# Kernel tuning notes

Hardware: AMD Instinct MI355X
Metric: run time of the kernel (lower is better)

Reference implementation:

```python
import jax, jax.numpy as jnp
import numpy as np

B, L, D = 4, 2048, 512
DK = D // 2
DH = 256.0  # scaling denominator


def _skew(QE):
    # QE: [B, L, M] with M == L (relative position logits via skewing trick)
    b, l, m = QE.shape
    pad = jnp.zeros((b, l, 1), QE.dtype)
    cat = jnp.concatenate([pad, QE], axis=2)      # [B, L, M+1]
    reshaped = cat.reshape(b, m + 1, l)           # [B, M+1, L]
    return reshaped[:, 1:, :]                     # [B, M, L]


def setup_inputs() -> dict:
    key = jax.random.key(0)
    ks = jax.random.split(key, 7)
    return {
        "inputQ": jax.random.normal(ks[0], (B, L, D), jnp.float32),
        "inputK": jax.random.normal(ks[1], (B, L, D), jnp.float32),
        "inputV": jax.random.normal(ks[2], (B, L, D), jnp.float32),
        "Wq": jax.random.normal(ks[3], (D, DK), jnp.float32) * 0.02,
        "Wk": jax.random.normal(ks[4], (D, DK), jnp.float32) * 0.02,
        "Wv": jax.random.normal(ks[5], (D, D), jnp.float32) * 0.02,
        "E": jax.random.normal(ks[6], (L, DK), jnp.float32) * 0.02,
    }


def reference(inputQ, inputK, inputV, Wq, Wk, Wv, E):
    Q = jnp.einsum('bld,dk->blk', inputQ, Wq)   # [B, L, DK]
    K = jnp.einsum('bld,dk->blk', inputK, Wk)   # [B, L, DK]
    V = jnp.einsum('bld,de->ble', inputV, Wv)   # [B, L, D]
    QE = jnp.einsum('blk,mk->blm', Q, E)        # [B, L, max_seq]
    Srel = _skew(QE)                             # [B, L, L]
    QKt = jnp.einsum('blk,bmk->blm', Q, K)      # [B, L, L]
    attn = jax.nn.softmax((QKt + Srel) / jnp.sqrt(jnp.float32(DH)), axis=-1)
    return jnp.einsum('blm,bme->ble', attn, V)  # [B, L, D]
```

## Files before the change

### kernel.cpp

```cpp
#include <hip/hip_runtime.h>
#include <hip/hip_bf16.h>

#define BB 4
#define LL 2048
#define DD 512
#define DKK 256

typedef __bf16 bf16;
typedef __bf16 bf16x4 __attribute__((ext_vector_type(4)));
typedef __bf16 bf16x8 __attribute__((ext_vector_type(8)));
typedef float f32x4 __attribute__((ext_vector_type(4)));

__device__ __forceinline__ void async_ld16(const bf16* g, bf16* l) {
    __builtin_amdgcn_global_load_lds(
        (const __attribute__((address_space(1))) void*)g,
        (__attribute__((address_space(3))) void*)l, 16, 0, 0);
}

__global__ void conv3_f32_bf16(const float* __restrict__ a, const float* __restrict__ bq,
                               const float* __restrict__ c,
                               bf16* __restrict__ oa, bf16* __restrict__ ob,
                               bf16* __restrict__ oc, int n4) {
    const float* in = (blockIdx.y == 0) ? a : (blockIdx.y == 1) ? bq : c;
    bf16* out = (blockIdx.y == 0) ? oa : (blockIdx.y == 1) ? ob : oc;
    int i = blockIdx.x * 256 + threadIdx.x;
    if (i < n4) {
        f32x4 v = *(const f32x4*)(in + (size_t)i * 4);
        bf16x4 o;
        #pragma unroll
        for (int j = 0; j < 4; ++j) o[j] = (bf16)v[j];
        *(bf16x4*)(out + (size_t)i * 4) = o;
    }
}

__global__ void prep_misc(const float* __restrict__ E, const float* __restrict__ Wq,
                          const float* __restrict__ Wk, const float* __restrict__ Wv,
                          bf16* __restrict__ Eb, bf16* __restrict__ WqT,
                          bf16* __restrict__ WkT, bf16* __restrict__ WvT) {
    int y = blockIdx.y;
    int idx = blockIdx.x * 256 + threadIdx.x;
    if (y == 0) {
        if (idx < (LL * DKK) / 4) {
            f32x4 v = *(const f32x4*)(E + (size_t)idx * 4);
            bf16x4 o;
            #pragma unroll
            for (int j = 0; j < 4; ++j) o[j] = (bf16)v[j];
            *(bf16x4*)(Eb + (size_t)idx * 4) = o;
        }
    } else if (y == 1) {
        if (idx < DD * DKK) { int r = idx / DKK, c = idx % DKK; WqT[(size_t)c * DD + r] = (bf16)Wq[idx]; }
    } else if (y == 2) {
        if (idx < DD * DKK) { int r = idx / DKK, c = idx % DKK; WkT[(size_t)c * DD + r] = (bf16)Wk[idx]; }
    } else {
        if (idx < DD * DD)  { int r = idx / DD,  c = idx % DD;  WvT[(size_t)c * DD + r] = (bf16)Wv[idx]; }
    }
}

__launch_bounds__(256, 2)
__global__ void gemm_qkv(const bf16* __restrict__ Xq, const bf16* __restrict__ WqT,
                         bf16* __restrict__ Qw,
                         const bf16* __restrict__ Xk, const bf16* __restrict__ WkT,
                         bf16* __restrict__ Kw,
                         const bf16* __restrict__ Xv, const bf16* __restrict__ WvT,
                         bf16* __restrict__ Vt)
{
    __shared__ bf16 Als[2][128 * 32];
    __shared__ bf16 Bls[2][128 * 32];
    __shared__ bf16 tbuf[64 * 136];

    int tid  = threadIdx.x;
    int lane = tid & 63;
    int wid  = tid >> 6;
    int l15  = lane & 15;
    int quad = lane >> 4;

    int bid  = blockIdx.x;
    int mode = (bid < 128) ? 0 : (bid < 256) ? 1 : 2;
    int idx  = bid - ((mode == 0) ? 0 : (mode == 1) ? 128 : 256);
    int nb   = (mode == 2) ? 4 : 2;
    int gx = idx % nb;
    int gy = idx / nb;
    int N  = (mode == 2) ? DD : DKK;
    const bf16* A  = (mode == 0) ? Xq  : (mode == 1) ? Xk  : Xv;
    const bf16* Bw = (mode == 0) ? WqT : (mode == 1) ? WkT : WvT;
    const int K = DD;

    const bf16* Ab = A + (size_t)gy * 128 * K;
    const bf16* Bb = Bw + (size_t)gx * 128 * K;

    int rl = lane >> 2;
    int sl = lane & 3;
    int half = wid & 1;
    const bf16* gsrc = (wid < 2) ? Ab : Bb;
    bf16* ldst0 = (wid < 2) ? Als[0] : Bls[0];
    bf16* ldst1 = (wid < 2) ? Als[1] : Bls[1];

    const bf16* gptr[4];
    #pragma unroll
    for (int u = 0; u < 4; ++u) {
        int inst = half * 4 + u;
        int row  = inst * 16 + rl;
        int c    = (sl - (row >> 1)) & 3;
        gptr[u] = gsrc + (size_t)row * K + c * 8;
    }

    f32x4 acc[4][4];
    #pragma unroll
    for (int i = 0; i < 4; ++i)
        #pragma unroll
        for (int j = 0; j < 4; ++j) acc[i][j] = 0;

    for (int k0 = 0; k0 < K; k0 += 64) {
        #pragma unroll
        for (int u = 0; u < 4; ++u) {
            async_ld16(gptr[u],      ldst0 + (half * 4 + u) * 512);
            async_ld16(gptr[u] + 32, ldst1 + (half * 4 + u) * 512);
            gptr[u] += 64;
        }
        __syncthreads();
        #pragma unroll
        for (int h2 = 0; h2 < 2; ++h2) {
            bf16x8 fA[4], fB[4];
            #pragma unroll
            for (int rt = 0; rt < 4; ++rt) {
                int row = (wid & 1) * 64 + rt * 16 + l15;
                int s   = (quad + (row >> 1)) & 3;
                fA[rt] = *(const bf16x8*)&Als[h2][row * 32 + s * 8];
            }
            #pragma unroll
            for (int ct = 0; ct < 4; ++ct) {
                int col = (wid >> 1) * 64 + ct * 16 + l15;
                int s   = (quad + (col >> 1)) & 3;
                fB[ct] = *(const bf16x8*)&Bls[h2][col * 32 + s * 8];
            }
            #pragma unroll
            for (int rt = 0; rt < 4; ++rt)
                #pragma unroll
                for (int ct = 0; ct < 4; ++ct)
                    acc[rt][ct] = __builtin_amdgcn_mfma_f32_16x16x32_bf16(
                                      fA[rt], fB[ct], acc[rt][ct], 0, 0, 0);
        }
        __syncthreads();
    }

    if (mode == 2) {
        #pragma unroll
        for (int p = 0; p < 2; ++p) {
            if ((wid >> 1) == p) {
                #pragma unroll
                for (int rt = 0; rt < 4; ++rt)
                    #pragma unroll
                    for (int ct = 0; ct < 4; ++ct)
                        #pragma unroll
                        for (int r = 0; r < 4; ++r)
                            tbuf[(ct * 16 + l15) * 136
                                 + (wid & 1) * 64 + rt * 16 + quad * 4 + r]
                                = (bf16)acc[rt][ct][r];
            }
            __syncthreads();
            int row = tid >> 2, c0 = (tid & 3) * 32;
            bf16* dst = Vt + (size_t)(gx * 128 + p * 64 + row) * (BB * LL)
                           + (size_t)gy * 128 + c0;
            #pragma unroll
            for (int q = 0; q < 4; ++q)
                *(bf16x8*)(dst + q * 8) = *(const bf16x8*)&tbuf[row * 136 + c0 + q * 8];
            __syncthreads();
        }
    } else {
        bf16* Cb = (mode == 0) ? Qw : Kw;
        int m0 = gy * 128 + (wid & 1) * 64;
        int n0 = gx * 128 + (wid >> 1) * 64;
        #pragma unroll
        for (int rt = 0; rt < 4; ++rt)
            #pragma unroll
            for (int ct = 0; ct < 4; ++ct)
                #pragma unroll
                for (int r = 0; r < 4; ++r) {
                    int m = m0 + rt * 16 + quad * 4 + r;
                    int n = n0 + ct * 16 + l15;
                    Cb[(size_t)m * N + n] = (bf16)acc[rt][ct][r];
                }
    }
}

__launch_bounds__(256, 2)
__global__ void gemm_srel(const bf16* __restrict__ A, const bf16* __restrict__ B,
                          bf16* __restrict__ C, long aStride, long cStride)
{
    __shared__ bf16 Als[2][128 * 32];
    __shared__ bf16 Bls[2][128 * 32];

    int tid  = threadIdx.x;
    int lane = tid & 63;
    int wid  = tid >> 6;
    int l15  = lane & 15;
    int quad = lane >> 4;
    const int N = LL, K = DKK;
    int nb = N >> 7;
    int gx = blockIdx.x % nb;
    int gy = blockIdx.x / nb;

    const bf16* Ab = A + (size_t)blockIdx.y * aStride + (size_t)gy * 128 * K;
    const bf16* Bb = B + (size_t)gx * 128 * K;

    int rl = lane >> 2;
    int sl = lane & 3;
    int half = wid & 1;
    const bf16* gsrc = (wid < 2) ? Ab : Bb;
    bf16* ldst0 = (wid < 2) ? Als[0] : Bls[0];
    bf16* ldst1 = (wid < 2) ? Als[1] : Bls[1];

    const bf16* gptr[4];
    #pragma unroll
    for (int u = 0; u < 4; ++u) {
        int inst = half * 4 + u;
        int row  = inst * 16 + rl;
        int c    = (sl - (row >> 1)) & 3;
        gptr[u] = gsrc + (size_t)row * K + c * 8;
    }

    f32x4 acc[4][4];
    #pragma unroll
    for (int i = 0; i < 4; ++i)
        #pragma unroll
        for (int j = 0; j < 4; ++j) acc[i][j] = 0;

    for (int k0 = 0; k0 < K; k0 += 64) {
        #pragma unroll
        for (int u = 0; u < 4; ++u) {
            async_ld16(gptr[u],      ldst0 + (half * 4 + u) * 512);
            async_ld16(gptr[u] + 32, ldst1 + (half * 4 + u) * 512);
            gptr[u] += 64;
        }
        __syncthreads();
        #pragma unroll
        for (int h2 = 0; h2 < 2; ++h2) {
            bf16x8 fA[4], fB[4];
            #pragma unroll
            for (int rt = 0; rt < 4; ++rt) {
                int row = (wid & 1) * 64 + rt * 16 + l15;
                int s   = (quad + (row >> 1)) & 3;
                fA[rt] = *(const bf16x8*)&Als[h2][row * 32 + s * 8];
            }
            #pragma unroll
            for (int ct = 0; ct < 4; ++ct) {
                int col = (wid >> 1) * 64 + ct * 16 + l15;
                int s   = (quad + (col >> 1)) & 3;
                fB[ct] = *(const bf16x8*)&Bls[h2][col * 32 + s * 8];
            }
            #pragma unroll
            for (int rt = 0; rt < 4; ++rt)
                #pragma unroll
                for (int ct = 0; ct < 4; ++ct)
                    acc[rt][ct] = __builtin_amdgcn_mfma_f32_16x16x32_bf16(
                                      fA[rt], fB[ct], acc[rt][ct], 0, 0, 0);
        }
        __syncthreads();
    }

    bf16* Cb = C + (size_t)blockIdx.y * cStride;
    int m0 = gy * 128 + (wid & 1) * 64;
    int n0 = gx * 128 + (wid >> 1) * 64;
    #pragma unroll
    for (int rt = 0; rt < 4; ++rt)
        #pragma unroll
        for (int ct = 0; ct < 4; ++ct)
            #pragma unroll
            for (int r = 0; r < 4; ++r) {
                int row = m0 + rt * 16 + quad * 4 + r;
                int c   = n0 + ct * 16 + l15;
                bool lower = (c >= LL - 1 - row);
                int dr = lower ? row : row - 1;
                int dc = lower ? c - (LL - 1 - row) : c + row + 1;
                if (lower || row >= 1)
                    Cb[(size_t)dr * LL + dc] = (bf16)acc[rt][ct][r];
            }
}

__launch_bounds__(256, 2)
__global__ void attn_kernel(const bf16* __restrict__ Qw, const bf16* __restrict__ Kw,
                            const bf16* __restrict__ Vt, const bf16* __restrict__ Srel,
                            float* __restrict__ out)
{
    __shared__ bf16  Klds[64 * 256];
    __shared__ bf16  Vlds[256 * 64];
    __shared__ float Ss[32][68];
    __shared__ bf16  Ps[32][72];
    __shared__ float mSt[32], lSt[32], aSt[32];

    int tid  = threadIdx.x;
    int lane = tid & 63;
    int wid  = tid >> 6;
    int l15  = lane & 15;
    int quad = lane >> 4;

    int xcd = blockIdx.x & 7;
    int b   = xcd >> 1;
    int dh  = xcd & 1;
    int i0  = (blockIdx.x >> 3) * 32;

    const bf16* Qb = Qw + (size_t)b * LL * DKK;
    const bf16* Kb = Kw + (size_t)b * LL * DKK;
    const bf16* Sb = Srel + (size_t)b * LL * LL;
    const bf16* Vb = Vt + (size_t)(dh * 256) * (BB * LL) + (size_t)b * LL;

    const bf16* kptr[8];
    const bf16* vptr[8];
    #pragma unroll
    for (int u = 0; u < 8; ++u) {
        int inst = wid * 8 + u;
        int j_ = inst * 2 + (lane >> 5);
        int ck = ((lane & 31) - j_) & 31;
        kptr[u] = Kb + (size_t)j_ * DKK + ck * 8;
        int d_ = inst * 8 + (lane >> 3);
        int cv = ((lane & 7) - d_) & 7;
        vptr[u] = Vb + (size_t)d_ * (BB * LL) + cv * 8;
    }

    bf16x8 Qreg[2][8];
    #pragma unroll
    for (int rt = 0; rt < 2; ++rt)
        #pragma unroll
        for (int ks = 0; ks < 8; ++ks)
            Qreg[rt][ks] = *(const bf16x8*)(Qb + (size_t)(i0 + rt * 16 + l15) * DKK
                                            + ks * 32 + quad * 8);

    if (tid < 32) { mSt[tid] = -1e30f; lSt[tid] = 0.f; }

    f32x4 accO[2][4];
    #pragma unroll
    for (int rt = 0; rt < 2; ++rt)
        #pragma unroll
        for (int nt = 0; nt < 4; ++nt) accO[rt][nt] = 0;

    asm volatile("s_waitcnt vmcnt(0)" ::: "memory");

    #pragma unroll
    for (int u = 0; u < 8; ++u) {
        async_ld16(kptr[u], Klds + (wid * 8 + u) * 512);
        kptr[u] += 64 * DKK;
    }
    __builtin_amdgcn_sched_barrier(0);
    int srow = i0 + (tid >> 3), ssg = tid & 7;
    bf16x8 srelCur = *(const bf16x8*)(Sb + (size_t)srow * LL + ssg * 8);
    const bf16* sPtr = Sb + (size_t)srow * LL + ssg * 8 + 64;
    __builtin_amdgcn_sched_barrier(0);
    #pragma unroll
    for (int u = 0; u < 8; ++u) {
        async_ld16(vptr[u], Vlds + (wid * 8 + u) * 512);
        vptr[u] += 64;
    }

    int jrow = wid * 16 + l15;

    for (int j0 = 0; j0 < LL; j0 += 64) {
        bool notlast = (j0 + 64 < LL);

        asm volatile("s_waitcnt vmcnt(9)" ::: "memory");
        bf16x8 kf[8];
        #pragma unroll
        for (int ks = 0; ks < 8; ++ks) {
            int cp = (ks * 4 + quad + jrow) & 31;
            kf[ks] = *(const bf16x8*)&Klds[jrow * 256 + cp * 8];
        }
        asm volatile("s_waitcnt lgkmcnt(0)" ::: "memory");
        __builtin_amdgcn_sched_barrier(0);
        if (notlast) {
            #pragma unroll
            for (int u = 0; u < 8; ++u) {
                async_ld16(kptr[u], Klds + (wid * 8 + u) * 512);
                kptr[u] += 64 * DKK;
            }
        }
        __builtin_amdgcn_sched_barrier(0);
        bf16x8 srelNext;
        if (notlast) {
            srelNext = *(const bf16x8*)sPtr;
            sPtr += 64;
        }
        __builtin_amdgcn_sched_barrier(0);
        f32x4 s0 = 0, s1 = 0;
        __builtin_amdgcn_s_setprio(1);
        #pragma unroll
        for (int ks = 0; ks < 8; ++ks) {
            s0 = __builtin_amdgcn_mfma_f32_16x16x32_bf16(Qreg[0][ks], kf[ks], s0, 0, 0, 0);
            s1 = __builtin_amdgcn_mfma_f32_16x16x32_bf16(Qreg[1][ks], kf[ks], s1, 0, 0, 0);
        }
        __builtin_amdgcn_s_setprio(0);
        #pragma unroll
        for (int r = 0; r < 4; ++r) {
            Ss[quad * 4 + r][wid * 16 + l15]      = s0[r];
            Ss[16 + quad * 4 + r][wid * 16 + l15] = s1[r];
        }
        asm volatile("s_waitcnt lgkmcnt(0)\ns_barrier" ::: "memory");

        {
            int r = tid >> 3, sg = tid & 7;
            int i = i0 + r;
            float v[8];
            #pragma unroll
            for (int c = 0; c < 8; ++c) {
                float sr = (j0 + sg * 8 + c == i + 1) ? 0.f : (float)srelCur[c];
                v[c] = (Ss[r][sg * 8 + c] + sr) * 0.0625f;
            }
            float tmax = v[0];
            #pragma unroll
            for (int c = 1; c < 8; ++c) tmax = fmaxf(tmax, v[c]);
            tmax = fmaxf(tmax, __shfl_xor(tmax, 1));
            tmax = fmaxf(tmax, __shfl_xor(tmax, 2));
            tmax = fmaxf(tmax, __shfl_xor(tmax, 4));
            float mOld = mSt[r], lOld = lSt[r];
            float mNew = fmaxf(mOld, tmax);
            float alpha = __expf(mOld - mNew);
            float ps = 0.f;
            bf16x8 pv;
            #pragma unroll
            for (int c = 0; c < 8; ++c) {
                float p = __expf(v[c] - mNew);
                ps += p;
                pv[c] = (bf16)p;
            }
            ps += __shfl_xor(ps, 1);
            ps += __shfl_xor(ps, 2);
            ps += __shfl_xor(ps, 4);
            *(bf16x8*)&Ps[r][sg * 8] = pv;
            if (sg == 0) { mSt[r] = mNew; lSt[r] = alpha * lOld + ps; aSt[r] = alpha; }
        }
        srelCur = srelNext;
        asm volatile("s_waitcnt lgkmcnt(0)\ns_barrier" ::: "memory");

        if (notlast) asm volatile("s_waitcnt vmcnt(9)" ::: "memory");
        else         asm volatile("s_waitcnt vmcnt(0)" ::: "memory");
        bf16x8 aF[2][2];
        #pragma unroll
        for (int rt = 0; rt < 2; ++rt)
            #pragma unroll
            for (int kk = 0; kk < 2; ++kk)
                aF[rt][kk] = *(const bf16x8*)&Ps[rt * 16 + l15][kk * 32 + quad * 8];
        float ar[2][4];
        #pragma unroll
        for (int rt = 0; rt < 2; ++rt)
            #pragma unroll
            for (int r = 0; r < 4; ++r) ar[rt][r] = aSt[rt * 16 + quad * 4 + r];
        bf16x8 vf[4][2];
        #pragma unroll
        for (int nt = 0; nt < 4; ++nt) {
            int dd = wid * 64 + nt * 16 + l15;
            int c0 = (quad + dd) & 7;
            int c1 = (4 + quad + dd) & 7;
            vf[nt][0] = *(const bf16x8*)&Vlds[dd * 64 + c0 * 8];
            vf[nt][1] = *(const bf16x8*)&Vlds[dd * 64 + c1 * 8];
        }
        asm volatile("s_waitcnt lgkmcnt(0)" ::: "memory");
        __builtin_amdgcn_sched_barrier(0);
        if (notlast) {
            #pragma unroll
            for (int u = 0; u < 8; ++u) {
                async_ld16(vptr[u], Vlds + (wid * 8 + u) * 512);
                vptr[u] += 64;
            }
        }
        __builtin_amdgcn_sched_barrier(0);
        __builtin_amdgcn_s_setprio(1);
        #pragma unroll
        for (int nt = 0; nt < 4; ++nt) {
            #pragma unroll
            for (int rt = 0; rt < 2; ++rt) {
                f32x4 o = accO[rt][nt];
                o[0] *= ar[rt][0]; o[1] *= ar[rt][1];
                o[2] *= ar[rt][2]; o[3] *= ar[rt][3];
                o = __builtin_amdgcn_mfma_f32_16x16x32_bf16(aF[rt][0], vf[nt][0], o, 0, 0, 0);
                o = __builtin_amdgcn_mfma_f32_16x16x32_bf16(aF[rt][1], vf[nt][1], o, 0, 0, 0);
                accO[rt][nt] = o;
            }
        }
        __builtin_amdgcn_s_setprio(0);
    }
    float lr[2][4];
    #pragma unroll
    for (int rt = 0; rt < 2; ++rt)
        #pragma unroll
        for (int r = 0; r < 4; ++r) lr[rt][r] = 1.f / lSt[rt * 16 + quad * 4 + r];
    #pragma unroll
    for (int rt = 0; rt < 2; ++rt)
        #pragma unroll
        for (int nt = 0; nt < 4; ++nt)
            #pragma unroll
            for (int r = 0; r < 4; ++r) {
                int i = i0 + rt * 16 + quad * 4 + r;
                int d = dh * 256 + wid * 64 + nt * 16 + l15;
                out[((size_t)b * LL + i) * DD + d] = accO[rt][nt][r] * lr[rt][r];
            }
}

extern "C" void kernel_launch(void* const* d_in, const int* in_sizes, int n_in,
                              void* d_out, int out_size, void* d_ws, size_t ws_size,
                              hipStream_t stream) {
    const float* inQ = (const float*)d_in[0];
    const float* inK = (const float*)d_in[1];
    const float* inV = (const float*)d_in[2];
    const float* Wq  = (const float*)d_in[3];
    const float* Wk  = (const float*)d_in[4];
    const float* Wv  = (const float*)d_in[5];
    const float* E   = (const float*)d_in[6];
    float* out = (float*)d_out;

    char* ws = (char*)d_ws;
    bf16* Qw   = (bf16*)(ws);
    bf16* Kw   = (bf16*)(ws + ((size_t)4  << 20));
    bf16* Vt   = (bf16*)(ws + ((size_t)8  << 20));
    bf16* SrelW= (bf16*)(ws + ((size_t)16 << 20));
    bf16* Xq   = (bf16*)(ws + ((size_t)16 << 20));
    bf16* Xk   = (bf16*)(ws + ((size_t)24 << 20));
    bf16* Xv   = (bf16*)(ws + ((size_t)32 << 20));
    bf16* WqT  = (bf16*)(ws + ((size_t)48 << 20));
    bf16* WkT  = (bf16*)(ws + ((size_t)48 << 20) + 262144);
    bf16* WvT  = (bf16*)(ws + ((size_t)48 << 20) + 524288);
    bf16* Eb   = (bf16*)(ws + ((size_t)49 << 20));

    conv3_f32_bf16<<<dim3(4096, 3), 256, 0, stream>>>(inQ, inK, inV, Xq, Xk, Xv,
                                                      (BB * LL * DD) / 4);
    prep_misc<<<dim3(1024, 4), 256, 0, stream>>>(E, Wq, Wk, Wv, Eb, WqT, WkT, WvT);

    gemm_qkv<<<512, 256, 0, stream>>>(Xq, WqT, Qw, Xk, WkT, Kw, Xv, WvT, Vt);
    gemm_srel<<<dim3(16 * 16, BB), 256, 0, stream>>>(Qw, Eb, SrelW,
                                                     (long)LL * DKK, (long)LL * LL);
    attn_kernel<<<dim3(BB * 64 * 2), 256, 0, stream>>>(Qw, Kw, Vt, SrelW, out);
}
```

Before: 221.7 us.

## Double-buffer LDS in projection and Srel GEMMs; merge prep kernels into one launch

The QKV and Srel GEMMs now use two LDS stages, so the async global-to-LDS load for the next K-slice is issued before the MFMA work on the current slice, and one barrier per step is removed. The two conversion/transpose prep kernels are combined into a single launch that dispatches on block index. This roughly doubles LDS use per block (the V transpose buffer now aliases the A stage buffer), which may lower occupancy. Correctness depends on the async LDS loads having landed by the next barrier.

Result: faster. 211.6 us (-4.5%).

```diff
diff --git a/kernel.cpp b/kernel.cpp
--- a/kernel.cpp
+++ b/kernel.cpp
@@ -17,42 +17,46 @@
         (__attribute__((address_space(3))) void*)l, 16, 0, 0);
 }
 
-__global__ void conv3_f32_bf16(const float* __restrict__ a, const float* __restrict__ bq,
-                               const float* __restrict__ c,
-                               bf16* __restrict__ oa, bf16* __restrict__ ob,
-                               bf16* __restrict__ oc, int n4) {
-    const float* in = (blockIdx.y == 0) ? a : (blockIdx.y == 1) ? bq : c;
-    bf16* out = (blockIdx.y == 0) ? oa : (blockIdx.y == 1) ? ob : oc;
-    int i = blockIdx.x * 256 + threadIdx.x;
-    if (i < n4) {
+__global__ void prep_all(const float* __restrict__ inQ, const float* __restrict__ inK,
+                         const float* __restrict__ inV, const float* __restrict__ E,
+                         const float* __restrict__ Wq, const float* __restrict__ Wk,
+                         const float* __restrict__ Wv,
+                         bf16* __restrict__ Xq, bf16* __restrict__ Xk,
+                         bf16* __restrict__ Xv, bf16* __restrict__ Eb,
+                         bf16* __restrict__ WqT, bf16* __restrict__ WkT,
+                         bf16* __restrict__ WvT)
+{
+    int bid = blockIdx.x;
+    int t = threadIdx.x;
+    if (bid < 12288) {
+        int region = bid >> 12;
+        int i = (bid & 4095) * 256 + t;
+        const float* in = (region == 0) ? inQ : (region == 1) ? inK : inV;
+        bf16* out = (region == 0) ? Xq : (region == 1) ? Xk : Xv;
         f32x4 v = *(const f32x4*)(in + (size_t)i * 4);
         bf16x4 o;
         #pragma unroll
         for (int j = 0; j < 4; ++j) o[j] = (bf16)v[j];
         *(bf16x4*)(out + (size_t)i * 4) = o;
-    }
-}
-
-__global__ void prep_misc(const float* __restrict__ E, const float* __restrict__ Wq,
-                          const float* __restrict__ Wk, const float* __restrict__ Wv,
-                          bf16* __restrict__ Eb, bf16* __restrict__ WqT,
-                          bf16* __restrict__ WkT, bf16* __restrict__ WvT) {
-    int y = blockIdx.y;
-    int idx = blockIdx.x * 256 + threadIdx.x;
-    if (y == 0) {
-        if (idx < (LL * DKK) / 4) {
-            f32x4 v = *(const f32x4*)(E + (size_t)idx * 4);
-            bf16x4 o;
-            #pragma unroll
-            for (int j = 0; j < 4; ++j) o[j] = (bf16)v[j];
-            *(bf16x4*)(Eb + (size_t)idx * 4) = o;
-        }
-    } else if (y == 1) {
-        if (idx < DD * DKK) { int r = idx / DKK, c = idx % DKK; WqT[(size_t)c * DD + r] = (bf16)Wq[idx]; }
-    } else if (y == 2) {
-        if (idx < DD * DKK) { int r = idx / DKK, c = idx % DKK; WkT[(size_t)c * DD + r] = (bf16)Wk[idx]; }
+    } else if (bid < 12800) {
+        int i = (bid - 12288) * 256 + t;
+        f32x4 v = *(const f32x4*)(E + (size_t)i * 4);
+        bf16x4 o;
+        #pragma unroll
+        for (int j = 0; j < 4; ++j) o[j] = (bf16)v[j];
+        *(bf16x4*)(Eb + (size_t)i * 4) = o;
+    } else if (bid < 13312) {
+        int idx = (bid - 12800) * 256 + t;
+        int r = idx / DKK, c = idx % DKK;
+        WqT[(size_t)c * DD + r] = (bf16)Wq[idx];
+    } else if (bid < 13824) {
+        int idx = (bid - 13312) * 256 + t;
+        int r = idx / DKK, c = idx % DKK;
+        WkT[(size_t)c * DD + r] = (bf16)Wk[idx];
     } else {
-        if (idx < DD * DD)  { int r = idx / DD,  c = idx % DD;  WvT[(size_t)c * DD + r] = (bf16)Wv[idx]; }
+        int idx = (bid - 13824) * 256 + t;
+        int r = idx / DD, c = idx % DD;
+        WvT[(size_t)c * DD + r] = (bf16)Wv[idx];
     }
 }
 
@@ -64,9 +68,8 @@
                          const bf16* __restrict__ Xv, const bf16* __restrict__ WvT,
                          bf16* __restrict__ Vt)
 {
-    __shared__ bf16 Als[2][128 * 32];
-    __shared__ bf16 Bls[2][128 * 32];
-    __shared__ bf16 tbuf[64 * 136];
+    __shared__ bf16 Als[2][2][128 * 32];
+    __shared__ bf16 Bls[2][2][128 * 32];
 
     int tid  = threadIdx.x;
     int lane = tid & 63;
@@ -92,8 +95,7 @@
     int sl = lane & 3;
     int half = wid & 1;
     const bf16* gsrc = (wid < 2) ? Ab : Bb;
-    bf16* ldst0 = (wid < 2) ? Als[0] : Bls[0];
-    bf16* ldst1 = (wid < 2) ? Als[1] : Bls[1];
+    bf16 (*ls)[2][128 * 32] = (wid < 2) ? Als : Bls;
 
     const bf16* gptr[4];
     #pragma unroll
@@ -104,34 +106,40 @@
         gptr[u] = gsrc + (size_t)row * K + c * 8;
     }
 
+#define STAGE_G(P) do {                                                    \
+    _Pragma("unroll")                                                      \
+    for (int u_ = 0; u_ < 4; ++u_) {                                       \
+        async_ld16(gptr[u_],      &ls[P][0][(half * 4 + u_) * 512]);       \
+        async_ld16(gptr[u_] + 32, &ls[P][1][(half * 4 + u_) * 512]);       \
+        gptr[u_] += 64;                                                    \
+    } } while (0)
+
     f32x4 acc[4][4];
     #pragma unroll
     for (int i = 0; i < 4; ++i)
         #pragma unroll
         for (int j = 0; j < 4; ++j) acc[i][j] = 0;
 
-    for (int k0 = 0; k0 < K; k0 += 64) {
-        #pragma unroll
-        for (int u = 0; u < 4; ++u) {
-            async_ld16(gptr[u],      ldst0 + (half * 4 + u) * 512);
-            async_ld16(gptr[u] + 32, ldst1 + (half * 4 + u) * 512);
-            gptr[u] += 64;
-        }
-        __syncthreads();
+    const int nsteps = K / 64;
+    STAGE_G(0);
+    __syncthreads();
+    for (int s = 0; s < nsteps; ++s) {
+        int cur = s & 1;
+        if (s + 1 < nsteps) STAGE_G(cur ^ 1);
         #pragma unroll
         for (int h2 = 0; h2 < 2; ++h2) {
             bf16x8 fA[4], fB[4];
             #pragma unroll
             for (int rt = 0; rt < 4; ++rt) {
                 int row = (wid & 1) * 64 + rt * 16 + l15;
-                int s   = (quad + (row >> 1)) & 3;
-                fA[rt] = *(const bf16x8*)&Als[h2][row * 32 + s * 8];
+                int sx  = (quad + (row >> 1)) & 3;
+                fA[rt] = *(const bf16x8*)&Als[cur][h2][row * 32 + sx * 8];
             }
             #pragma unroll
             for (int ct = 0; ct < 4; ++ct) {
                 int col = (wid >> 1) * 64 + ct * 16 + l15;
-                int s   = (quad + (col >> 1)) & 3;
-                fB[ct] = *(const bf16x8*)&Bls[h2][col * 32 + s * 8];
+                int sx  = (quad + (col >> 1)) & 3;
+                fB[ct] = *(const bf16x8*)&Bls[cur][h2][col * 32 + sx * 8];
             }
             #pragma unroll
             for (int rt = 0; rt < 4; ++rt)
@@ -140,10 +148,12 @@
                     acc[rt][ct] = __builtin_amdgcn_mfma_f32_16x16x32_bf16(
                                       fA[rt], fB[ct], acc[rt][ct], 0, 0, 0);
         }
-        __syncthreads();
-    }
+        if (s + 1 < nsteps || mode == 2) __syncthreads();
+    }
+#undef STAGE_G
 
     if (mode == 2) {
+        bf16* tbuf = &Als[0][0][0];
         #pragma unroll
         for (int p = 0; p < 2; ++p) {
             if ((wid >> 1) == p) {
@@ -187,8 +197,8 @@
 __global__ void gemm_srel(const bf16* __restrict__ A, const bf16* __restrict__ B,
                           bf16* __restrict__ C, long aStride, long cStride)
 {
-    __shared__ bf16 Als[2][128 * 32];
-    __shared__ bf16 Bls[2][128 * 32];
+    __shared__ bf16 Als[2][2][128 * 32];
+    __shared__ bf16 Bls[2][2][128 * 32];
 
     int tid  = threadIdx.x;
     int lane = tid & 63;
@@ -207,8 +217,7 @@
     int sl = lane & 3;
     int half = wid & 1;
     const bf16* gsrc = (wid < 2) ? Ab : Bb;
-    bf16* ldst0 = (wid < 2) ? Als[0] : Bls[0];
-    bf16* ldst1 = (wid < 2) ? Als[1] : Bls[1];
+    bf16 (*ls)[2][128 * 32] = (wid < 2) ? Als : Bls;
 
     const bf16* gptr[4];
     #pragma unroll
@@ -219,34 +228,40 @@
         gptr[u] = gsrc + (size_t)row * K + c * 8;
     }
 
+#define STAGE_S(P) do {                                                    \
+    _Pragma("unroll")                                                      \
+    for (int u_ = 0; u_ < 4; ++u_) {                                       \
+        async_ld16(gptr[u_],      &ls[P][0][(half * 4 + u_) * 512]);       \
+        async_ld16(gptr[u_] + 32, &ls[P][1][(half * 4 + u_) * 512]);       \
+        gptr[u_] += 64;                                                    \
+    } } while (0)
+
     f32x4 acc[4][4];
     #pragma unroll
     for (int i = 0; i < 4; ++i)
         #pragma unroll
         for (int j = 0; j < 4; ++j) acc[i][j] = 0;
 
-    for (int k0 = 0; k0 < K; k0 += 64) {
-        #pragma unroll
-        for (int u = 0; u < 4; ++u) {
-            async_ld16(gptr[u],      ldst0 + (half * 4 + u) * 512);
-            async_ld16(gptr[u] + 32, ldst1 + (half * 4 + u) * 512);
-            gptr[u] += 64;
-        }
-        __syncthreads();
+    const int nsteps = K / 64;
+    STAGE_S(0);
+    __syncthreads();
+    for (int s = 0; s < nsteps; ++s) {
+        int cur = s & 1;
+        if (s + 1 < nsteps) STAGE_S(cur ^ 1);
         #pragma unroll
         for (int h2 = 0; h2 < 2; ++h2) {
             bf16x8 fA[4], fB[4];
             #pragma unroll
             for (int rt = 0; rt < 4; ++rt) {
                 int row = (wid & 1) * 64 + rt * 16 + l15;
-                int s   = (quad + (row >> 1)) & 3;
-                fA[rt] = *(const bf16x8*)&Als[h2][row * 32 + s * 8];
+                int sx  = (quad + (row >> 1)) & 3;
+                fA[rt] = *(const bf16x8*)&Als[cur][h2][row * 32 + sx * 8];
             }
             #pragma unroll
             for (int ct = 0; ct < 4; ++ct) {
                 int col = (wid >> 1) * 64 + ct * 16 + l15;
-                int s   = (quad + (col >> 1)) & 3;
-                fB[ct] = *(const bf16x8*)&Bls[h2][col * 32 + s * 8];
+                int sx  = (quad + (col >> 1)) & 3;
+                fB[ct] = *(const bf16x8*)&Bls[cur][h2][col * 32 + sx * 8];
             }
             #pragma unroll
             for (int rt = 0; rt < 4; ++rt)
@@ -255,8 +270,9 @@
                     acc[rt][ct] = __builtin_amdgcn_mfma_f32_16x16x32_bf16(
                                       fA[rt], fB[ct], acc[rt][ct], 0, 0, 0);
         }
-        __syncthreads();
-    }
+        if (s + 1 < nsteps) __syncthreads();
+    }
+#undef STAGE_S
 
     bf16* Cb = C + (size_t)blockIdx.y * cStride;
     int m0 = gy * 128 + (wid & 1) * 64;
@@ -518,10 +534,8 @@
     bf16* WvT  = (bf16*)(ws + ((size_t)48 << 20) + 524288);
     bf16* Eb   = (bf16*)(ws + ((size_t)49 << 20));
 
-    conv3_f32_bf16<<<dim3(4096, 3), 256, 0, stream>>>(inQ, inK, inV, Xq, Xk, Xv,
-                                                      (BB * LL * DD) / 4);
-    prep_misc<<<dim3(1024, 4), 256, 0, stream>>>(E, Wq, Wk, Wv, Eb, WqT, WkT, WvT);
-
+    prep_all<<<14848, 256, 0, stream>>>(inQ, inK, inV, E, Wq, Wk, Wv,
+                                        Xq, Xk, Xv, Eb, WqT, WkT, WvT);
     gemm_qkv<<<512, 256, 0, stream>>>(Xq, WqT, Qw, Xk, WkT, Kw, Xv, WvT, Vt);
     gemm_srel<<<dim3(16 * 16, BB), 256, 0, stream>>>(Qw, Eb, SrelW,
                                                      (long)LL * DKK, (long)LL * LL);
```
